# Kernel tuning notes

Hardware: AMD Instinct MI355X
Metric: run time of the kernel (lower is better)

## Reference

```python
import jax, jax.numpy as jnp
import numpy as np

# Mamba2 dims (defaults: expand=2, d_state=128, d_conv=4, ngroups=1)
D_MODEL = 1024
HEADDIM = 64
D_STATE = 128
D_CONV = 4
D_INNER = 2 * D_MODEL            # 2048
NHEADS = D_INNER // HEADDIM      # 32
CONV_DIM = D_INNER + 2 * D_STATE # 2304
D_IN_PROJ = 2 * D_INNER + 2 * D_STATE + NHEADS  # 4384
EPS = 1e-5


def setup_inputs() -> dict:
    key = jax.random.key(0)
    ks = jax.random.split(key, 12)
    B, L = 4, 2048
    inp = {}
    inp['query'] = jax.random.normal(ks[0], (B, L, D_MODEL), jnp.float32)
    inp['key'] = jax.random.normal(ks[1], (B, L, D_MODEL), jnp.float32)
    inp['value'] = jax.random.normal(ks[2], (B, L, D_MODEL), jnp.float32)
    # parameters (Mamba2-style init)
    inp['in_proj_w'] = jax.random.normal(ks[3], (D_IN_PROJ, D_MODEL), jnp.float32) * (D_MODEL ** -0.5)
    inp['conv_w'] = jax.random.normal(ks[4], (CONV_DIM, D_CONV), jnp.float32) * (D_CONV ** -0.5)
    inp['conv_b'] = jnp.zeros((CONV_DIM,), jnp.float32)
    # dt init: softplus^{-1}(dt) with dt ~ U[1e-3, 1e-1]
    dt = jnp.exp(jax.random.uniform(ks[5], (NHEADS,)) * (np.log(0.1) - np.log(1e-3)) + np.log(1e-3))
    inp['dt_bias'] = dt + jnp.log(-jnp.expm1(-dt))
    # A ~ U[1, 16], A_log = log(A)
    inp['A_log'] = jnp.log(jax.random.uniform(ks[6], (NHEADS,), minval=1.0, maxval=16.0))
    inp['D'] = jnp.ones((NHEADS,), jnp.float32)
    inp['norm_w'] = jnp.ones((D_INNER,), jnp.float32)
    inp['out_proj_w'] = jax.random.normal(ks[7], (D_MODEL, D_INNER), jnp.float32) * (D_INNER ** -0.5)
    return inp


def _mamba2_forward(u, in_proj_w, conv_w, conv_b, dt_bias, A_log, D, norm_w, out_proj_w):
    b, l, _ = u.shape
    zxbcdt = jnp.einsum('bld,ed->ble', u, in_proj_w)  # (b,l,D_IN_PROJ)
    z = zxbcdt[..., :D_INNER]
    xBC = zxbcdt[..., D_INNER:D_INNER + CONV_DIM]
    dt = jax.nn.softplus(zxbcdt[..., -NHEADS:] + dt_bias)  # (b,l,h)
    # depthwise causal conv1d over time, kernel D_CONV, + silu
    xBC_pad = jnp.pad(xBC, ((0, 0), (D_CONV - 1, 0), (0, 0)))
    conv = conv_b
    for k in range(D_CONV):
        conv = conv + xBC_pad[:, k:k + l, :] * conv_w[:, k]
    xBC = jax.nn.silu(conv)
    x = xBC[..., :D_INNER].reshape(b, l, NHEADS, HEADDIM)   # (b,l,h,p)
    Bm = xBC[..., D_INNER:D_INNER + D_STATE]                # (b,l,n) ngroups=1
    Cm = xBC[..., D_INNER + D_STATE:]                       # (b,l,n)
    A = -jnp.exp(A_log)                                      # (h,)
    dA = jnp.exp(dt * A)                                     # (b,l,h)

    def step(h, inputs):
        dA_t, dt_t, x_t, B_t, C_t = inputs  # (b,h),(b,h),(b,h,p),(b,n),(b,n)
        h = h * dA_t[:, :, None, None] + (dt_t[:, :, None, None] * x_t[..., None]) * B_t[:, None, None, :]
        y = jnp.einsum('bhpn,bn->bhp', h, C_t)
        return h, y

    h0 = jnp.zeros((b, NHEADS, HEADDIM, D_STATE), u.dtype)
    xs = (dA.transpose(1, 0, 2), dt.transpose(1, 0, 2), x.transpose(1, 0, 2, 3),
          Bm.transpose(1, 0, 2), Cm.transpose(1, 0, 2))
    _, ys = jax.lax.scan(step, h0, xs)
    y = ys.transpose(1, 0, 2, 3) + x * D[None, None, :, None]  # (b,l,h,p)
    y = y.reshape(b, l, D_INNER)
    # RMSNormGated (norm_before_gate=False): norm(y * silu(z)) * w
    y = y * jax.nn.silu(z)
    y = y * jax.lax.rsqrt(jnp.mean(y * y, axis=-1, keepdims=True) + EPS) * norm_w
    return jnp.einsum('ble,de->bld', y, out_proj_w)


def reference(query, key, value, in_proj_w, conv_w, conv_b, dt_bias, A_log, D, norm_w, out_proj_w):
    # wrapper ignores key/value; returns mamba(query) (cache pass-through omitted)
    return _mamba2_forward(query, in_proj_w, conv_w, conv_b, dt_bias, A_log, D, norm_w, out_proj_w)
```

## Files before the change

kernel.cpp:

```cpp
#include <hip/hip_runtime.h>
#include <hip/hip_bf16.h>


typedef __attribute__((ext_vector_type(8))) short bf16x8;
typedef __attribute__((ext_vector_type(4))) float f32x4;

static constexpr int B_ = 4;
static constexpr int L_ = 2048;
static constexpr int NROWS = B_ * L_;
static constexpr int DMODEL = 1024;
static constexpr int DINNER = 2048;
static constexpr int NH = 32;
static constexpr int DSTATE = 128;
static constexpr int CONVDIM = DINNER + 2 * DSTATE;
static constexpr int DINPROJ = 2 * DINNER + 2 * DSTATE + NH;
static constexpr int Q_ = 64;
static constexpr int NCHUNK = L_ / Q_;

__device__ __forceinline__ unsigned pk_bf16(float a, float b) {
  unsigned ua = __builtin_bit_cast(unsigned, a);
  unsigned ub = __builtin_bit_cast(unsigned, b);
  ua = (ua + 0x7FFFu + ((ua >> 16) & 1u)) >> 16;
  ub = (ub + 0x7FFFu + ((ub >> 16) & 1u)) >> 16;
  return (ua & 0xFFFFu) | (ub << 16);
}
__device__ __forceinline__ unsigned short bf16_of(float a) {
  unsigned ua = __builtin_bit_cast(unsigned, a);
  return (unsigned short)((ua + 0x7FFFu + ((ua >> 16) & 1u)) >> 16);
}
__device__ __forceinline__ float f_of_bf16(unsigned short s) {
  return __builtin_bit_cast(float, (unsigned)s << 16);
}
__device__ __forceinline__ unsigned short* state_slot(unsigned short* lo,
                                                      unsigned short* hi,
                                                      int bh, int c) {
  int i = bh * NCHUNK + c;
  return (i < 2048) ? lo + (size_t)i * 8192 : hi + (size_t)(i - 2048) * 8192;
}

__global__ __launch_bounds__(256) void cast4_kernel(const float* __restrict__ in,
                                                    unsigned short* __restrict__ out) {
  int i = blockIdx.x * 256 + threadIdx.x;
  float4 v = ((const float4*)in)[i];
  ((uint2*)out)[i] = make_uint2(pk_bf16(v.x, v.y), pk_bf16(v.z, v.w));
}

template <bool C_BF16>
__global__ __launch_bounds__(256) void gemm_lds_kernel(
    const unsigned short* __restrict__ A, const unsigned short* __restrict__ Bw,
    void* __restrict__ Cp, int M, int N, int K, int lda, int ldb, int ldc) {
  __shared__ unsigned short sA[128 * 32];
  __shared__ unsigned short sB[128 * 32];
  const int tid = threadIdx.x;
  const int w = tid >> 6;
  const int lane = tid & 63;
  const int m0 = blockIdx.y * 128;
  const int n0 = blockIdx.x * 128;
  const int wm = (w >> 1) * 64;
  const int wn = (w & 1) * 64;
  const int lr = lane >> 2;
  const int lc8 = (lane & 3) * 8;

  f32x4 acc[4][4];
#pragma unroll
  for (int i = 0; i < 4; ++i)
#pragma unroll
    for (int j = 0; j < 4; ++j) acc[i][j] = f32x4{0.f, 0.f, 0.f, 0.f};

  auto ldsA = (__attribute__((address_space(3))) unsigned short*)sA;
  auto ldsB = (__attribute__((address_space(3))) unsigned short*)sB;

  for (int k0 = 0; k0 < K; k0 += 32) {
#pragma unroll
    for (int s = 0; s < 2; ++s) {
      int row = w * 32 + s * 16;
      __builtin_amdgcn_global_load_lds(
          (const __attribute__((address_space(1))) void*)(A + (size_t)(m0 + row + lr) * lda + k0 + lc8),
          (__attribute__((address_space(3))) void*)(ldsA + row * 32), 16, 0, 0);
      __builtin_amdgcn_global_load_lds(
          (const __attribute__((address_space(1))) void*)(Bw + (size_t)(n0 + row + lr) * ldb + k0 + lc8),
          (__attribute__((address_space(3))) void*)(ldsB + row * 32), 16, 0, 0);
    }
    __syncthreads();
    const int k8 = (lane >> 4) * 8;
    const int r15 = lane & 15;
    bf16x8 af[4], bfr[4];
#pragma unroll
    for (int i = 0; i < 4; ++i)
      af[i] = *(const bf16x8*)(sA + (wm + i * 16 + r15) * 32 + k8);
#pragma unroll
    for (int j = 0; j < 4; ++j)
      bfr[j] = *(const bf16x8*)(sB + (wn + j * 16 + r15) * 32 + k8);
#pragma unroll
    for (int i = 0; i < 4; ++i)
#pragma unroll
      for (int j = 0; j < 4; ++j)
        acc[i][j] = __builtin_amdgcn_mfma_f32_16x16x32_bf16(af[i], bfr[j], acc[i][j], 0, 0, 0);
    __syncthreads();
  }

  const int rr = (lane >> 4) * 4;
  const int cc = lane & 15;
#pragma unroll
  for (int i = 0; i < 4; ++i) {
#pragma unroll
    for (int j = 0; j < 4; ++j) {
      int gcol = n0 + wn + j * 16 + cc;
      if (gcol < N) {
#pragma unroll
        for (int r = 0; r < 4; ++r) {
          size_t grow = (size_t)(m0 + wm + i * 16 + rr + r);
          if constexpr (C_BF16)
            ((unsigned short*)Cp)[grow * ldc + gcol] = bf16_of(acc[i][j][r]);
          else
            ((float*)Cp)[grow * ldc + gcol] = acc[i][j][r];
        }
      }
    }
  }
}

__global__ __launch_bounds__(256) void conv_kernel(const unsigned short* __restrict__ zx,
                                                   const float* __restrict__ conv_w,
                                                   const float* __restrict__ conv_b,
                                                   unsigned short* __restrict__ xbc) {
  int c = blockIdx.x * 256 + threadIdx.x;
  int row = blockIdx.y;
  int l = row & (L_ - 1);
  float acc = conv_b[c];
#pragma unroll
  for (int k = 0; k < 4; ++k) {
    int ll = l + k - 3;
    if (ll >= 0)
      acc = fmaf(f_of_bf16(zx[(size_t)(row + k - 3) * DINPROJ + DINNER + c]),
                 conv_w[c * 4 + k], acc);
  }
  acc = acc / (1.f + __expf(-acc));
  xbc[(size_t)row * CONVDIM + c] = bf16_of(acc);
}

__global__ __launch_bounds__(256) void dt_kernel(const unsigned short* __restrict__ zx,
                                                 const float* __restrict__ dt_bias,
                                                 float* __restrict__ dtv) {
  int i = blockIdx.x * 256 + threadIdx.x;
  int hh = i & (NH - 1);
  int row = i >> 5;
  float x = f_of_bf16(zx[(size_t)row * DINPROJ + DINNER + CONVDIM + hh]) + dt_bias[hh];
  dtv[i] = (x > 20.f) ? x : log1pf(__expf(x));
}

__global__ __launch_bounds__(256) void ssd_passA(unsigned short* __restrict__ xbc,
                                                 const float* __restrict__ dtv,
                                                 const float* __restrict__ A_log,
                                                 const float* __restrict__ Dvec,
                                                 unsigned short* __restrict__ st_lo,
                                                 unsigned short* __restrict__ st_hi) {
  const int bid = blockIdx.x;
  const int h = bid & 31;
  const int c = (bid >> 5) & 31;
  const int b = bid >> 10;
  const int bh = b * 32 + h;
  const int tid = threadIdx.x;
  const int w = tid >> 6;
  const int lane = tid & 63;
  const int quad = lane >> 4;
  const int c15 = lane & 15;

  __shared__ unsigned short sXt[64 * 72];
  __shared__ unsigned short sBq[64 * 136];
  __shared__ unsigned short sCB[128 * 72];
  __shared__ float sdt[64], scs[64], sg[64];

  const float A = -__expf(A_log[h]);
  const float Dh = Dvec[h];
  const int r0 = b * L_ + c * Q_;

  if (w == 0) {
    float v = dtv[(size_t)(r0 + lane) * NH + h];
    sdt[lane] = v;
    float s = v;
#pragma unroll
    for (int off = 1; off < 64; off <<= 1) {
      float t = __shfl_up(s, off, 64);
      if (lane >= off) s += t;
    }
    scs[lane] = s;
    float T = __shfl(s, 63, 64);
    sg[lane] = __expf(A * (T - s)) * v;
  }
  for (int e = tid; e < 512; e += 256) {
    int t = e & 63, pb = e >> 6;
    uint4 v = *(const uint4*)&xbc[(size_t)(r0 + t) * CONVDIM + h * 64 + pb * 8];
    const unsigned short* sv = (const unsigned short*)&v;
#pragma unroll
    for (int j = 0; j < 8; ++j) sXt[(pb * 8 + j) * 72 + t] = sv[j];
  }
  for (int e = tid; e < 1024; e += 256) {
    int s = e >> 4, ch = e & 15;
    size_t roff = (size_t)(r0 + s) * CONVDIM + DINNER;
    *(uint4*)&sBq[s * 136 + ch * 8] = *(const uint4*)&xbc[roff + ch * 8];
    *(uint4*)&sCB[s * 136 + ch * 8] = *(const uint4*)&xbc[roff + DSTATE + ch * 8];
  }
  __syncthreads();

  const int wt = w >> 1, wx = w & 1;
  f32x4 sacc[2][2];
#pragma unroll
  for (int i = 0; i < 2; ++i)
#pragma unroll
    for (int j = 0; j < 2; ++j) sacc[i][j] = f32x4{0.f, 0.f, 0.f, 0.f};
#pragma unroll
  for (int kk = 0; kk < 4; ++kk) {
    int k8 = quad * 8 + kk * 32;
    bf16x8 a0 = *(const bf16x8*)&sCB[(wt * 32 + c15) * 136 + k8];
    bf16x8 a1 = *(const bf16x8*)&sCB[(wt * 32 + 16 + c15) * 136 + k8];
    bf16x8 b0 = *(const bf16x8*)&sBq[(wx * 32 + c15) * 136 + k8];
    bf16x8 b1 = *(const bf16x8*)&sBq[(wx * 32 + 16 + c15) * 136 + k8];
    sacc[0][0] = __builtin_amdgcn_mfma_f32_16x16x32_bf16(a0, b0, sacc[0][0], 0, 0, 0);
    sacc[0][1] = __builtin_amdgcn_mfma_f32_16x16x32_bf16(a0, b1, sacc[0][1], 0, 0, 0);
    sacc[1][0] = __builtin_amdgcn_mfma_f32_16x16x32_bf16(a1, b0, sacc[1][0], 0, 0, 0);
    sacc[1][1] = __builtin_amdgcn_mfma_f32_16x16x32_bf16(a1, b1, sacc[1][1], 0, 0, 0);
  }
  __syncthreads();

#pragma unroll
  for (int i = 0; i < 2; ++i)
#pragma unroll
    for (int j = 0; j < 2; ++j) {
      int scol = wx * 32 + j * 16 + c15;
      float css = scs[scol], dts = sdt[scol];
#pragma unroll
      for (int r = 0; r < 4; ++r) {
        int trow = wt * 32 + i * 16 + quad * 4 + r;
        float v = (scol <= trow) ? sacc[i][j][r] * __expf(A * (scs[trow] - css)) * dts : 0.f;
        sBq[trow * 72 + scol] = bf16_of(v);
      }
    }
  for (int e = tid; e < 1024; e += 256) {
    int s = e & 63, nb = e >> 6;
    uint4 v = *(const uint4*)&xbc[(size_t)(r0 + s) * CONVDIM + DINNER + nb * 8];
    float g = sg[s];
    const unsigned short* sv = (const unsigned short*)&v;
#pragma unroll
    for (int j = 0; j < 8; ++j)
      sCB[(nb * 8 + j) * 72 + s] = bf16_of(f_of_bf16(sv[j]) * g);
  }
  __syncthreads();

  f32x4 yacc[2][2];
#pragma unroll
  for (int i = 0; i < 2; ++i)
#pragma unroll
    for (int j = 0; j < 2; ++j) yacc[i][j] = f32x4{0.f, 0.f, 0.f, 0.f};
#pragma unroll
  for (int kk = 0; kk < 2; ++kk) {
    int k8 = quad * 8 + kk * 32;
    bf16x8 a0 = *(const bf16x8*)&sBq[(wt * 32 + c15) * 72 + k8];
    bf16x8 a1 = *(const bf16x8*)&sBq[(wt * 32 + 16 + c15) * 72 + k8];
    bf16x8 b0 = *(const bf16x8*)&sXt[(wx * 32 + c15) * 72 + k8];
    bf16x8 b1 = *(const bf16x8*)&sXt[(wx * 32 + 16 + c15) * 72 + k8];
    yacc[0][0] = __builtin_amdgcn_mfma_f32_16x16x32_bf16(a0, b0, yacc[0][0], 0, 0, 0);
    yacc[0][1] = __builtin_amdgcn_mfma_f32_16x16x32_bf16(a0, b1, yacc[0][1], 0, 0, 0);
    yacc[1][0] = __builtin_amdgcn_mfma_f32_16x16x32_bf16(a1, b0, yacc[1][0], 0, 0, 0);
    yacc[1][1] = __builtin_amdgcn_mfma_f32_16x16x32_bf16(a1, b1, yacc[1][1], 0, 0, 0);
  }
#pragma unroll
  for (int i = 0; i < 2; ++i)
#pragma unroll
    for (int j = 0; j < 2; ++j) {
      int p = wx * 32 + j * 16 + c15;
#pragma unroll
      for (int r = 0; r < 4; ++r) {
        int t = wt * 32 + i * 16 + quad * 4 + r;
        float xv = f_of_bf16(sXt[p * 72 + t]);
        xbc[(size_t)(r0 + t) * CONVDIM + h * 64 + p] = bf16_of(yacc[i][j][r] + Dh * xv);
      }
    }

  f32x4 hacc[2][4];
#pragma unroll
  for (int i = 0; i < 2; ++i)
#pragma unroll
    for (int j = 0; j < 4; ++j) hacc[i][j] = f32x4{0.f, 0.f, 0.f, 0.f};
  const int wp = w >> 1, wn = w & 1;
#pragma unroll
  for (int kk = 0; kk < 2; ++kk) {
    int k8 = quad * 8 + kk * 32;
    bf16x8 a0 = *(const bf16x8*)&sXt[(wp * 32 + c15) * 72 + k8];
    bf16x8 a1 = *(const bf16x8*)&sXt[(wp * 32 + 16 + c15) * 72 + k8];
    bf16x8 bfr[4];
#pragma unroll
    for (int j = 0; j < 4; ++j)
      bfr[j] = *(const bf16x8*)&sCB[(wn * 64 + j * 16 + c15) * 72 + k8];
#pragma unroll
    for (int j = 0; j < 4; ++j) {
      hacc[0][j] = __builtin_amdgcn_mfma_f32_16x16x32_bf16(a0, bfr[j], hacc[0][j], 0, 0, 0);
      hacc[1][j] = __builtin_amdgcn_mfma_f32_16x16x32_bf16(a1, bfr[j], hacc[1][j], 0, 0, 0);
    }
  }
  unsigned short* slot = state_slot(st_lo, st_hi, bh, c);
#pragma unroll
  for (int i = 0; i < 2; ++i)
#pragma unroll
    for (int j = 0; j < 4; ++j)
#pragma unroll
      for (int r = 0; r < 4; ++r) {
        int p = wp * 32 + i * 16 + quad * 4 + r;
        int n = wn * 64 + j * 16 + c15;
        slot[p * 128 + n] = bf16_of(hacc[i][j][r]);
      }
}

__global__ __launch_bounds__(256) void ssd_passB(const float* __restrict__ dtv,
                                                 const float* __restrict__ A_log,
                                                 unsigned short* __restrict__ st_lo,
                                                 unsigned short* __restrict__ st_hi) {
  const int bh = blockIdx.x >> 1;
  const int ph = blockIdx.x & 1;
  const int h = bh & 31;
  const int b = bh >> 5;
  const int tid = threadIdx.x;
  __shared__ float sd[NCHUNK];
  const float A = -__expf(A_log[h]);
  if (tid < NCHUNK) {
    float s = 0.f;
    const float* dp = dtv + (size_t)(b * L_ + tid * Q_) * NH + h;
    for (int i = 0; i < Q_; ++i) s += dp[(size_t)i * NH];
    sd[tid] = __expf(A * s);
  }
  __syncthreads();
  float hreg[16];
#pragma unroll
  for (int k = 0; k < 16; ++k) hreg[k] = 0.f;
  const size_t eoff = (size_t)ph * 4096 + (size_t)tid * 16;
  for (int c = 0; c < NCHUNK; ++c) {
    unsigned short* sp = state_slot(st_lo, st_hi, bh, c) + eoff;
    uint4 t0 = ((const uint4*)sp)[0];
    uint4 t1 = ((const uint4*)sp)[1];
    unsigned o[8];
#pragma unroll
    for (int k = 0; k < 8; ++k) o[k] = pk_bf16(hreg[2 * k], hreg[2 * k + 1]);
    ((uint4*)sp)[0] = make_uint4(o[0], o[1], o[2], o[3]);
    ((uint4*)sp)[1] = make_uint4(o[4], o[5], o[6], o[7]);
    float d = sd[c];
    const unsigned short* tv0 = (const unsigned short*)&t0;
    const unsigned short* tv1 = (const unsigned short*)&t1;
#pragma unroll
    for (int k = 0; k < 8; ++k) hreg[k] = d * hreg[k] + f_of_bf16(tv0[k]);
#pragma unroll
    for (int k = 0; k < 8; ++k) hreg[8 + k] = d * hreg[8 + k] + f_of_bf16(tv1[k]);
  }
}

__global__ __launch_bounds__(256) void ssd_passC(unsigned short* __restrict__ xbc,
                                                 const float* __restrict__ dtv,
                                                 const float* __restrict__ A_log,
                                                 const unsigned short* __restrict__ st_lo,
                                                 const unsigned short* __restrict__ st_hi) {
  const int bid = blockIdx.x;
  const int h = bid & 31;
  const int c = (bid >> 5) & 31;
  const int b = bid >> 10;
  const int bh = b * 32 + h;
  const int tid = threadIdx.x;
  const int w = tid >> 6;
  const int lane = tid & 63;
  const int quad = lane >> 4;
  const int c15 = lane & 15;

  __shared__ unsigned short sC[64 * 136];
  __shared__ unsigned short sH[64 * 136];
  __shared__ float srt[64];

  const float A = -__expf(A_log[h]);
  const int r0 = b * L_ + c * Q_;

  if (w == 0) {
    float v = dtv[(size_t)(r0 + lane) * NH + h];
    float s = v;
#pragma unroll
    for (int off = 1; off < 64; off <<= 1) {
      float t = __shfl_up(s, off, 64);
      if (lane >= off) s += t;
    }
    srt[lane] = __expf(A * s);
  }
  const unsigned short* slot =
      state_slot((unsigned short*)st_lo, (unsigned short*)st_hi, bh, c);
  for (int e = tid; e < 1024; e += 256) {
    int s = e >> 4, ch = e & 15;
    *(uint4*)&sC[s * 136 + ch * 8] =
        *(const uint4*)&xbc[(size_t)(r0 + s) * CONVDIM + DINNER + DSTATE + ch * 8];
    *(uint4*)&sH[s * 136 + ch * 8] = *(const uint4*)&slot[s * 128 + ch * 8];
  }
  __syncthreads();

  const int wt = w >> 1, wx = w & 1;
  f32x4 yacc[2][2];
#pragma unroll
  for (int i = 0; i < 2; ++i)
#pragma unroll
    for (int j = 0; j < 2; ++j) yacc[i][j] = f32x4{0.f, 0.f, 0.f, 0.f};
#pragma unroll
  for (int kk = 0; kk < 4; ++kk) {
    int k8 = quad * 8 + kk * 32;
    bf16x8 a0 = *(const bf16x8*)&sC[(wt * 32 + c15) * 136 + k8];
    bf16x8 a1 = *(const bf16x8*)&sC[(wt * 32 + 16 + c15) * 136 + k8];
    bf16x8 b0 = *(const bf16x8*)&sH[(wx * 32 + c15) * 136 + k8];
    bf16x8 b1 = *(const bf16x8*)&sH[(wx * 32 + 16 + c15) * 136 + k8];
    yacc[0][0] = __builtin_amdgcn_mfma_f32_16x16x32_bf16(a0, b0, yacc[0][0], 0, 0, 0);
    yacc[0][1] = __builtin_amdgcn_mfma_f32_16x16x32_bf16(a0, b1, yacc[0][1], 0, 0, 0);
    yacc[1][0] = __builtin_amdgcn_mfma_f32_16x16x32_bf16(a1, b0, yacc[1][0], 0, 0, 0);
    yacc[1][1] = __builtin_amdgcn_mfma_f32_16x16x32_bf16(a1, b1, yacc[1][1], 0, 0, 0);
  }
#pragma unroll
  for (int i = 0; i < 2; ++i)
#pragma unroll
    for (int j = 0; j < 2; ++j) {
      int p = wx * 32 + j * 16 + c15;
#pragma unroll
      for (int r = 0; r < 4; ++r) {
        int t = wt * 32 + i * 16 + quad * 4 + r;
        size_t ga = (size_t)(r0 + t) * CONVDIM + h * 64 + p;
        float v = yacc[i][j][r] * srt[t] + f_of_bf16(xbc[ga]);
        xbc[ga] = bf16_of(v);
      }
    }
}

__global__ __launch_bounds__(256) void norm_kernel(const unsigned short* __restrict__ y_in,
                                                   unsigned short* __restrict__ zxb,
                                                   const float* __restrict__ norm_w) {
  const int row = blockIdx.x;
  const int tid = threadIdx.x;
  float v[8];
  float ss = 0.f;
#pragma unroll
  for (int i = 0; i < 8; ++i) {
    int c = tid + i * 256;
    float yv = f_of_bf16(y_in[(size_t)row * CONVDIM + c]);
    float z = f_of_bf16(zxb[(size_t)row * DINPROJ + c]);
    yv *= z / (1.f + __expf(-z));
    v[i] = yv;
    ss = fmaf(yv, yv, ss);
  }
#pragma unroll
  for (int o = 32; o > 0; o >>= 1) ss += __shfl_down(ss, o, 64);
  __shared__ float sred[4];
  if ((tid & 63) == 0) sred[tid >> 6] = ss;
  __syncthreads();
  float tot = (sred[0] + sred[1]) + (sred[2] + sred[3]);
  float r = rsqrtf(tot * (1.f / (float)DINNER) + 1e-5f);
#pragma unroll
  for (int i = 0; i < 8; ++i) {
    int c = tid + i * 256;
    zxb[(size_t)row * DINPROJ + c] = bf16_of(v[i] * r * norm_w[c]);
  }
}

extern "C" void kernel_launch(void* const* d_in, const int* in_sizes, int n_in,
                              void* d_out, int out_size, void* d_ws, size_t ws_size,
                              hipStream_t stream) {
  (void)in_sizes; (void)n_in; (void)out_size;
  const float* u          = (const float*)d_in[0];
  const float* in_proj_w  = (const float*)d_in[3];
  const float* conv_w     = (const float*)d_in[4];
  const float* conv_b     = (const float*)d_in[5];
  const float* dt_bias    = (const float*)d_in[6];
  const float* A_log      = (const float*)d_in[7];
  const float* Dvec       = (const float*)d_in[8];
  const float* norm_w     = (const float*)d_in[9];
  const float* out_proj_w = (const float*)d_in[10];
  float* out = (float*)d_out;

  constexpr size_t SZ_ZX   = (size_t)NROWS * DINPROJ * 2;
  constexpr size_t SZ_XBC  = (size_t)NROWS * CONVDIM * 2;
  constexpr size_t SZ_DT   = (size_t)NROWS * NH * 4;
  constexpr size_t SZ_SHR  = 33554432;
  constexpr size_t SZ_WOUT = (size_t)DMODEL * DINNER * 2;
  constexpr size_t NEED = SZ_ZX + SZ_XBC + SZ_DT + SZ_SHR + SZ_WOUT;
  if (ws_size < NEED) return;

  char* p = (char*)d_ws;
  unsigned short* zxb  = (unsigned short*)p; p += SZ_ZX;
  unsigned short* xbc  = (unsigned short*)p; p += SZ_XBC;
  float* dtv           = (float*)p;          p += SZ_DT;
  char* shared_reg     = p;                  p += SZ_SHR;
  unsigned short* wout_bf = (unsigned short*)p;

  unsigned short* u_bf   = (unsigned short*)shared_reg;
  unsigned short* win_bf = (unsigned short*)(shared_reg + 16777216);
  unsigned short* st_lo  = (unsigned short*)d_out;
  unsigned short* st_hi  = (unsigned short*)shared_reg;

  cast4_kernel<<<(NROWS * DMODEL) / 1024, 256, 0, stream>>>(u, u_bf);
  cast4_kernel<<<(DINPROJ * DMODEL) / 1024, 256, 0, stream>>>(in_proj_w, win_bf);
  cast4_kernel<<<(DMODEL * DINNER) / 1024, 256, 0, stream>>>(out_proj_w, wout_bf);

  gemm_lds_kernel<true><<<dim3(35, 64), 256, 0, stream>>>(
      u_bf, win_bf, zxb, NROWS, DINPROJ, DMODEL, DMODEL, DMODEL, DINPROJ);
  conv_kernel<<<dim3(9, NROWS), 256, 0, stream>>>(zxb, conv_w, conv_b, xbc);
  dt_kernel<<<(NROWS * NH) / 256, 256, 0, stream>>>(zxb, dt_bias, dtv);

  ssd_passA<<<B_ * NCHUNK * NH, 256, 0, stream>>>(xbc, dtv, A_log, Dvec, st_lo, st_hi);
  ssd_passB<<<B_ * NH * 2, 256, 0, stream>>>(dtv, A_log, st_lo, st_hi);
  ssd_passC<<<B_ * NCHUNK * NH, 256, 0, stream>>>(xbc, dtv, A_log, st_lo, st_hi);

  norm_kernel<<<NROWS, 256, 0, stream>>>(xbc, zxb, norm_w);
  gemm_lds_kernel<false><<<dim3(8, 64), 256, 0, stream>>>(
      zxb, wout_bf, out, NROWS, DMODEL, DINNER, DINPROJ, DINNER, DMODEL);
}
```

Before: 520.5 us.

## Retile GEMMs with K=64, XCD-aware block mapping, fuse dt into conv, vectorize norm

```diff
diff --git a/kernel.cpp b/kernel.cpp
--- a/kernel.cpp
+++ b/kernel.cpp
@@ -45,64 +45,78 @@
   ((uint2*)out)[i] = make_uint2(pk_bf16(v.x, v.y), pk_bf16(v.z, v.w));
 }
 
-template <bool C_BF16>
+template <int MT, bool C_BF16>
 __global__ __launch_bounds__(256) void gemm_lds_kernel(
     const unsigned short* __restrict__ A, const unsigned short* __restrict__ Bw,
-    void* __restrict__ Cp, int M, int N, int K, int lda, int ldb, int ldc) {
-  __shared__ unsigned short sA[128 * 32];
-  __shared__ unsigned short sB[128 * 32];
+    void* __restrict__ Cp, int M, int N, int K, int lda, int ldb, int ldc,
+    int per_xcd) {
+  constexpr int IB = MT / 32;
+  __shared__ unsigned short sA[MT * 64];
+  __shared__ unsigned short sB[128 * 64];
   const int tid = threadIdx.x;
   const int w = tid >> 6;
   const int lane = tid & 63;
-  const int m0 = blockIdx.y * 128;
-  const int n0 = blockIdx.x * 128;
-  const int wm = (w >> 1) * 64;
+  const int bid = blockIdx.x;
+  const int xcd = bid & 7;
+  const int t = bid >> 3;
+  const int by = xcd * per_xcd + (t % per_xcd);
+  const int bx = t / per_xcd;
+  const int m0 = by * MT;
+  const int n0 = bx * 128;
+  const int wm = (w >> 1) * (MT / 2);
   const int wn = (w & 1) * 64;
-  const int lr = lane >> 2;
-  const int lc8 = (lane & 3) * 8;
-
-  f32x4 acc[4][4];
-#pragma unroll
-  for (int i = 0; i < 4; ++i)
+  const int lr = lane >> 3;
+  const int lc8 = (lane & 7) * 8;
+
+  f32x4 acc[IB][4];
+#pragma unroll
+  for (int i = 0; i < IB; ++i)
 #pragma unroll
     for (int j = 0; j < 4; ++j) acc[i][j] = f32x4{0.f, 0.f, 0.f, 0.f};
 
   auto ldsA = (__attribute__((address_space(3))) unsigned short*)sA;
   auto ldsB = (__attribute__((address_space(3))) unsigned short*)sB;
 
-  for (int k0 = 0; k0 < K; k0 += 32) {
-#pragma unroll
-    for (int s = 0; s < 2; ++s) {
-      int row = w * 32 + s * 16;
+  for (int k0 = 0; k0 < K; k0 += 64) {
+#pragma unroll
+    for (int s = 0; s < IB; ++s) {
+      int row = w * (MT / 4) + s * 8;
       __builtin_amdgcn_global_load_lds(
           (const __attribute__((address_space(1))) void*)(A + (size_t)(m0 + row + lr) * lda + k0 + lc8),
-          (__attribute__((address_space(3))) void*)(ldsA + row * 32), 16, 0, 0);
+          (__attribute__((address_space(3))) void*)(ldsA + row * 64), 16, 0, 0);
+    }
+#pragma unroll
+    for (int s = 0; s < 4; ++s) {
+      int row = w * 32 + s * 8;
       __builtin_amdgcn_global_load_lds(
           (const __attribute__((address_space(1))) void*)(Bw + (size_t)(n0 + row + lr) * ldb + k0 + lc8),
-          (__attribute__((address_space(3))) void*)(ldsB + row * 32), 16, 0, 0);
+          (__attribute__((address_space(3))) void*)(ldsB + row * 64), 16, 0, 0);
     }
     __syncthreads();
-    const int k8 = (lane >> 4) * 8;
     const int r15 = lane & 15;
-    bf16x8 af[4], bfr[4];
-#pragma unroll
-    for (int i = 0; i < 4; ++i)
-      af[i] = *(const bf16x8*)(sA + (wm + i * 16 + r15) * 32 + k8);
-#pragma unroll
-    for (int j = 0; j < 4; ++j)
-      bfr[j] = *(const bf16x8*)(sB + (wn + j * 16 + r15) * 32 + k8);
-#pragma unroll
-    for (int i = 0; i < 4; ++i)
+#pragma unroll
+    for (int kb = 0; kb < 2; ++kb) {
+      const int kcol = kb * 32 + (lane >> 4) * 8;
+      bf16x8 af[IB], bfr[4];
+#pragma unroll
+      for (int i = 0; i < IB; ++i)
+        af[i] = *(const bf16x8*)(sA + (wm + i * 16 + r15) * 64 + kcol);
 #pragma unroll
       for (int j = 0; j < 4; ++j)
-        acc[i][j] = __builtin_amdgcn_mfma_f32_16x16x32_bf16(af[i], bfr[j], acc[i][j], 0, 0, 0);
+        bfr[j] = *(const bf16x8*)(sB + (wn + j * 16 + r15) * 64 + kcol);
+#pragma unroll
+      for (int i = 0; i < IB; ++i)
+#pragma unroll
+        for (int j = 0; j < 4; ++j)
+          acc[i][j] = __builtin_amdgcn_mfma_f32_16x16x32_bf16(af[i], bfr[j], acc[i][j], 0, 0, 0);
+    }
     __syncthreads();
   }
 
-  const int rr = (lane >> 4) * 4;
+  const int rr = ((lane >> 4)) * 4;
   const int cc = lane & 15;
 #pragma unroll
-  for (int i = 0; i < 4; ++i) {
+  for (int i = 0; i < IB; ++i) {
 #pragma unroll
     for (int j = 0; j < 4; ++j) {
       int gcol = n0 + wn + j * 16 + cc;
@@ -120,10 +134,12 @@
   }
 }
 
-__global__ __launch_bounds__(256) void conv_kernel(const unsigned short* __restrict__ zx,
-                                                   const float* __restrict__ conv_w,
-                                                   const float* __restrict__ conv_b,
-                                                   unsigned short* __restrict__ xbc) {
+__global__ __launch_bounds__(256) void conv_dt_kernel(const unsigned short* __restrict__ zx,
+                                                      const float* __restrict__ conv_w,
+                                                      const float* __restrict__ conv_b,
+                                                      const float* __restrict__ dt_bias,
+                                                      unsigned short* __restrict__ xbc,
+                                                      float* __restrict__ dtv) {
   int c = blockIdx.x * 256 + threadIdx.x;
   int row = blockIdx.y;
   int l = row & (L_ - 1);
@@ -137,16 +153,11 @@
   }
   acc = acc / (1.f + __expf(-acc));
   xbc[(size_t)row * CONVDIM + c] = bf16_of(acc);
-}
-
-__global__ __launch_bounds__(256) void dt_kernel(const unsigned short* __restrict__ zx,
-                                                 const float* __restrict__ dt_bias,
-                                                 float* __restrict__ dtv) {
-  int i = blockIdx.x * 256 + threadIdx.x;
-  int hh = i & (NH - 1);
-  int row = i >> 5;
-  float x = f_of_bf16(zx[(size_t)row * DINPROJ + DINNER + CONVDIM + hh]) + dt_bias[hh];
-  dtv[i] = (x > 20.f) ? x : log1pf(__expf(x));
+  if (blockIdx.x == 0 && threadIdx.x < NH) {
+    int hh = threadIdx.x;
+    float x = f_of_bf16(zx[(size_t)row * DINPROJ + DINNER + CONVDIM + hh]) + dt_bias[hh];
+    dtv[(size_t)row * NH + hh] = (x > 20.f) ? x : log1pf(__expf(x));
+  }
 }
 
 __global__ __launch_bounds__(256) void ssd_passA(unsigned short* __restrict__ xbc,
@@ -247,6 +258,7 @@
   }
   __syncthreads();
 
+  unsigned short* sS = sBq;
   f32x4 yacc[2][2];
 #pragma unroll
   for (int i = 0; i < 2; ++i)
@@ -255,8 +267,8 @@
 #pragma unroll
   for (int kk = 0; kk < 2; ++kk) {
     int k8 = quad * 8 + kk * 32;
-    bf16x8 a0 = *(const bf16x8*)&sBq[(wt * 32 + c15) * 72 + k8];
-    bf16x8 a1 = *(const bf16x8*)&sBq[(wt * 32 + 16 + c15) * 72 + k8];
+    bf16x8 a0 = *(const bf16x8*)&sS[(wt * 32 + c15) * 72 + k8];
+    bf16x8 a1 = *(const bf16x8*)&sS[(wt * 32 + 16 + c15) * 72 + k8];
     bf16x8 b0 = *(const bf16x8*)&sXt[(wx * 32 + c15) * 72 + k8];
     bf16x8 b1 = *(const bf16x8*)&sXt[(wx * 32 + 16 + c15) * 72 + k8];
     yacc[0][0] = __builtin_amdgcn_mfma_f32_16x16x32_bf16(a0, b0, yacc[0][0], 0, 0, 0);
@@ -433,16 +445,20 @@
                                                    const float* __restrict__ norm_w) {
   const int row = blockIdx.x;
   const int tid = threadIdx.x;
+  const int c0 = tid * 8;
+  uint4 yv4 = *(const uint4*)&y_in[(size_t)row * CONVDIM + c0];
+  uint4 zv4 = *(const uint4*)&zxb[(size_t)row * DINPROJ + c0];
+  const unsigned short* yv = (const unsigned short*)&yv4;
+  const unsigned short* zv = (const unsigned short*)&zv4;
   float v[8];
   float ss = 0.f;
 #pragma unroll
   for (int i = 0; i < 8; ++i) {
-    int c = tid + i * 256;
-    float yv = f_of_bf16(y_in[(size_t)row * CONVDIM + c]);
-    float z = f_of_bf16(zxb[(size_t)row * DINPROJ + c]);
-    yv *= z / (1.f + __expf(-z));
-    v[i] = yv;
-    ss = fmaf(yv, yv, ss);
+    float yf = f_of_bf16(yv[i]);
+    float z = f_of_bf16(zv[i]);
+    yf *= z / (1.f + __expf(-z));
+    v[i] = yf;
+    ss = fmaf(yf, yf, ss);
   }
 #pragma unroll
   for (int o = 32; o > 0; o >>= 1) ss += __shfl_down(ss, o, 64);
@@ -451,11 +467,12 @@
   __syncthreads();
   float tot = (sred[0] + sred[1]) + (sred[2] + sred[3]);
   float r = rsqrtf(tot * (1.f / (float)DINNER) + 1e-5f);
-#pragma unroll
-  for (int i = 0; i < 8; ++i) {
-    int c = tid + i * 256;
-    zxb[(size_t)row * DINPROJ + c] = bf16_of(v[i] * r * norm_w[c]);
-  }
+  unsigned o4[4];
+#pragma unroll
+  for (int k = 0; k < 4; ++k)
+    o4[k] = pk_bf16(v[2 * k] * r * norm_w[c0 + 2 * k],
+                    v[2 * k + 1] * r * norm_w[c0 + 2 * k + 1]);
+  *(uint4*)&zxb[(size_t)row * DINPROJ + c0] = make_uint4(o4[0], o4[1], o4[2], o4[3]);
 }
 
 extern "C" void kernel_launch(void* const* d_in, const int* in_sizes, int n_in,
@@ -497,16 +514,16 @@
   cast4_kernel<<<(DINPROJ * DMODEL) / 1024, 256, 0, stream>>>(in_proj_w, win_bf);
   cast4_kernel<<<(DMODEL * DINNER) / 1024, 256, 0, stream>>>(out_proj_w, wout_bf);
 
-  gemm_lds_kernel<true><<<dim3(35, 64), 256, 0, stream>>>(
-      u_bf, win_bf, zxb, NROWS, DINPROJ, DMODEL, DMODEL, DMODEL, DINPROJ);
-  conv_kernel<<<dim3(9, NROWS), 256, 0, stream>>>(zxb, conv_w, conv_b, xbc);
-  dt_kernel<<<(NROWS * NH) / 256, 256, 0, stream>>>(zxb, dt_bias, dtv);
+  gemm_lds_kernel<128, true><<<2240, 256, 0, stream>>>(
+      u_bf, win_bf, zxb, NROWS, DINPROJ, DMODEL, DMODEL, DMODEL, DINPROJ, 8);
+  conv_dt_kernel<<<dim3(9, NROWS), 256, 0, stream>>>(zxb, conv_w, conv_b, dt_bias,
+                                                     xbc, dtv);
 
   ssd_passA<<<B_ * NCHUNK * NH, 256, 0, stream>>>(xbc, dtv, A_log, Dvec, st_lo, st_hi);
   ssd_passB<<<B_ * NH * 2, 256, 0, stream>>>(dtv, A_log, st_lo, st_hi);
   ssd_passC<<<B_ * NCHUNK * NH, 256, 0, stream>>>(xbc, dtv, A_log, st_lo, st_hi);
 
   norm_kernel<<<NROWS, 256, 0, stream>>>(xbc, zxb, norm_w);
-  gemm_lds_kernel<false><<<dim3(8, 64), 256, 0, stream>>>(
-      zxb, wout_bf, out, NROWS, DMODEL, DINNER, DINPROJ, DINNER, DMODEL);
-}
+  gemm_lds_kernel<64, false><<<1024, 256, 0, stream>>>(
+      zxb, wout_bf, out, NROWS, DMODEL, DINNER, DINPROJ, DINNER, DMODEL, 16);
+}
```

Result: no change. 525.3 us (+0.9%).
